# Optimization experiments

Measured on AMD Instinct MI355X. Metric: run time of the kernel, lower is better.

## Reference

```python
import jax, jax.numpy as jnp
import numpy as np

B, S = 256, 512
NQ = 1000           # n_skills
MEM, DK, DV, FC = 20, 50, 200, 50  # memory_size, key dim, value dim, final fc dim


def _kaiming(key, shape, fan_in):
    return jax.random.normal(key, shape) * np.float32(np.sqrt(2.0 / fan_in))


def setup_inputs() -> dict:
    key = jax.random.key(0)
    ks = jax.random.split(key, 12)
    q_data = jax.random.randint(ks[0], (B, S), 0, NQ + 1)
    qa_data = jax.random.randint(ks[1], (B, S), 0, 2 * NQ + 1)
    u = jax.random.uniform(ks[2], (B * S,))
    # target: -1 = masked/padding, else binary label (matches target.ge(0) masking)
    target = jnp.where(u < 0.1, -1.0, (u > 0.55).astype(jnp.float32))
    q_embed_w = _kaiming(ks[3], (NQ + 1, DK), DK)
    qa_embed_w = _kaiming(ks[4], (2 * NQ + 1, DV), DV)
    memory_key = _kaiming(ks[5], (MEM, DK), DK)
    init_memory_value = _kaiming(ks[6], (MEM, DV), DV)
    erase_w = _kaiming(ks[7], (DV, DV), DV)
    erase_b = jnp.zeros((DV,), jnp.float32)
    add_w = _kaiming(ks[8], (DV, DV), DV)
    add_b = jnp.zeros((DV,), jnp.float32)
    read_w = _kaiming(ks[9], (DV + FC, FC), DV + FC)
    read_b = jnp.zeros((FC,), jnp.float32)
    pred_w = _kaiming(ks[10], (FC, 1), FC)
    pred_b = jnp.zeros((1,), jnp.float32)
    return dict(q_data=q_data, qa_data=qa_data, target=target,
                q_embed_w=q_embed_w, qa_embed_w=qa_embed_w,
                memory_key=memory_key, init_memory_value=init_memory_value,
                erase_w=erase_w, erase_b=erase_b, add_w=add_w, add_b=add_b,
                read_w=read_w, read_b=read_b, pred_w=pred_w, pred_b=pred_b)


def reference(q_data, qa_data, target, q_embed_w, qa_embed_w, memory_key,
              init_memory_value, erase_w, erase_b, add_w, add_b,
              read_w, read_b, pred_w, pred_b):
    b = q_data.shape[0]
    q_e = q_embed_w[q_data]     # [B,S,DK]
    qa_e = qa_embed_w[qa_data]  # [B,S,DV]
    Mv0 = jnp.broadcast_to(init_memory_value, (b, MEM, DV))

    def step(Mv, xs):
        q_t, qa_t = xs                                        # [B,DK], [B,DV]
        corr = jax.nn.softmax(q_t @ memory_key.T, axis=1)     # [B,MEM] addressing
        read = jnp.einsum('bm,bmd->bd', corr, Mv)             # weighted read
        erase = jax.nn.sigmoid(qa_t @ erase_w + erase_b)      # [B,DV]
        add = jnp.tanh(qa_t @ add_w + add_b)                  # [B,DV]
        w = corr[:, :, None]                                  # [B,MEM,1]
        Mv = Mv * (1.0 - w * erase[:, None, :]) + w * add[:, None, :]
        return Mv, read

    _, reads = jax.lax.scan(step, Mv0, (q_e.transpose(1, 0, 2), qa_e.transpose(1, 0, 2)))
    reads = reads.transpose(1, 0, 2)                          # [B,S,DV]
    x = jnp.concatenate([reads, q_e], axis=-1)                # [B,S,DV+FC]
    h = jnp.tanh(x @ read_w + read_b)                         # [B,S,FC]
    logits = (h @ pred_w + pred_b).reshape(-1)                # [B*S]
    mask = target >= 0.0
    t = jnp.where(mask, target, 0.0)
    # numerically-stable BCE-with-logits, masked mean
    bce = jnp.maximum(logits, 0.0) - logits * t + jnp.log1p(jnp.exp(-jnp.abs(logits)))
    loss = jnp.sum(jnp.where(mask, bce, 0.0)) / jnp.maximum(mask.sum(), 1)
    return loss, jax.nn.sigmoid(logits)
```

## Files before the change

### kernel.cpp

```cpp
#include <hip/hip_runtime.h>
#include <math.h>

#define B_   256
#define S_   512
#define NQ_  1000
#define MEM_ 20
#define DK_  50
#define DV_  200
#define FC_  50
#define RPB  2
#define CHK  8
#define CLEN (S_/CHK)
#define HLEN 32
#define NKS  7
#define XS_STRIDE 232
#define CORR_STRIDE 12
#define NB_EA    ((2*NQ_+1+RPB-1)/RPB)
#define NB_CORR  4
#define NB_WPACK 7
#define NB_HQ    251
#define PREP_BLOCKS (NB_EA+NB_CORR+NB_WPACK+NB_HQ)
#define MM_BLOCKS (B_*CHK)
#define SCANA_BLOCKS (B_*(CHK-1))

typedef __attribute__((ext_vector_type(8))) short bf16x8_t;
typedef __attribute__((ext_vector_type(4))) float f32x4_t;
typedef __attribute__((ext_vector_type(2))) _Float16 f16x2_t;

static __device__ __forceinline__ f16x2_t h2(unsigned u){ return __builtin_bit_cast(f16x2_t, u); }
static __device__ __forceinline__ unsigned h2u(f16x2_t v){ return __builtin_bit_cast(unsigned, v); }
static __device__ __forceinline__ unsigned packh2(float x, float y){
  unsigned short bx = __builtin_bit_cast(unsigned short, (_Float16)x);
  unsigned short by = __builtin_bit_cast(unsigned short, (_Float16)y);
  return (unsigned)bx | ((unsigned)by << 16);
}
static __device__ __forceinline__ f16x2_t pkfma16(f16x2_t a, f16x2_t b, f16x2_t c){
  return __builtin_elementwise_fma(a, b, c);
}
static __device__ __forceinline__ f16x2_t splat_l(f16x2_t p){ return __builtin_shufflevector(p, p, 0, 0); }
static __device__ __forceinline__ f16x2_t splat_h(f16x2_t p){ return __builtin_shufflevector(p, p, 1, 1); }

static __device__ __forceinline__ unsigned short f2bf(float f){
  unsigned u = __float_as_uint(f);
  unsigned r = u + 0x7fffu + ((u >> 16) & 1u);
  return (unsigned short)(r >> 16);
}
static __device__ __forceinline__ float ftanh(float x){
  float e = __expf(2.f*x);
  return 1.f - 2.f*__builtin_amdgcn_rcpf(e+1.f);
}
static __device__ __forceinline__ float fsigm(float x){
  return __builtin_amdgcn_rcpf(1.f+__expf(-x));
}

__global__ __launch_bounds__(256) void k_prep1(
    const float* __restrict__ qaw,
    const float* __restrict__ ew, const float* __restrict__ eb,
    const float* __restrict__ aw, const float* __restrict__ ab,
    unsigned* __restrict__ eaTab,
    const float* __restrict__ qw, const float* __restrict__ mk,
    unsigned* __restrict__ corrH,
    const float* __restrict__ rw, const float* __restrict__ rb,
    const float* __restrict__ pw,
    unsigned short* __restrict__ WpFrag, float* __restrict__ pwPad,
    float* __restrict__ hq){
  __shared__ float qa[RPB*DV_];
  int blk = blockIdx.x;
  if(blk < NB_EA){
    int row0 = blk*RPB;
    for(int i=threadIdx.x; i<RPB*DV_; i+=256){
      int r = i/DV_, cc = i - r*DV_;
      int row = row0 + r;
      qa[i] = (row <= 2*NQ_) ? qaw[row*DV_+cc] : 0.f;
    }
    __syncthreads();
    int d = threadIdx.x;
    if(d >= DV_) return;
    float accE[RPB], accA[RPB];
    #pragma unroll
    for(int r=0;r<RPB;++r){ accE[r] = eb[d]; accA[r] = ab[d]; }
    float we0 = ew[d], wa0 = aw[d];
    for(int j=0;j<DV_;++j){
      int jn = (j+1 < DV_) ? j+1 : j;
      float we1 = ew[jn*DV_+d];
      float wa1 = aw[jn*DV_+d];
      #pragma unroll
      for(int r=0;r<RPB;++r){
        float x = qa[r*DV_+j];
        accE[r] = fmaf(x, we0, accE[r]);
        accA[r] = fmaf(x, wa0, accA[r]);
      }
      we0 = we1; wa0 = wa1;
    }
    #pragma unroll
    for(int r=0;r<RPB;++r){
      int row = row0 + r;
      if(row <= 2*NQ_){
        unsigned he = (unsigned)__builtin_bit_cast(unsigned short, (_Float16)fsigm(accE[r]));
        unsigned ha = (unsigned)__builtin_bit_cast(unsigned short, (_Float16)ftanh(accA[r]));
        eaTab[(size_t)row*DV_+d] = he | (ha << 16);
      }
    }
  } else if(blk < NB_EA+NB_CORR){
    int q = (blk-NB_EA)*256 + threadIdx.x;
    if(q > NQ_) return;
    float qv[DK_];
    #pragma unroll
    for(int j=0;j<DK_;++j) qv[j] = qw[q*DK_+j];
    float s[MEM_]; float mx = -1e30f;
    #pragma unroll
    for(int m=0;m<MEM_;++m){
      float acc = 0.f;
      #pragma unroll
      for(int j=0;j<DK_;++j) acc = fmaf(qv[j], mk[m*DK_+j], acc);
      s[m] = acc; mx = fmaxf(mx, acc);
    }
    float sum = 0.f;
    #pragma unroll
    for(int m=0;m<MEM_;++m){ s[m] = __expf(s[m]-mx); sum += s[m]; }
    float inv = __builtin_amdgcn_rcpf(sum);
    #pragma unroll
    for(int i=0;i<MEM_/2;++i)
      corrH[q*CORR_STRIDE+i] = packh2(s[2*i]*inv, s[2*i+1]*inv);
  } else if(blk < NB_EA+NB_CORR+NB_WPACK){
    int ks = blk - (NB_EA+NB_CORR);
    int nt = threadIdx.x >> 6;
    int lane = threadIdx.x & 63;
    int quad = lane >> 4, col = lane & 15;
    int n = nt*16 + col;
    unsigned short tmp[8];
    #pragma unroll
    for(int j=0;j<8;++j){
      int k = ks*32 + quad*8 + j;
      tmp[j] = (k < DV_ && n < FC_) ? f2bf(rw[k*FC_+n]) : (unsigned short)0;
    }
    uint4* dst = reinterpret_cast<uint4*>(WpFrag + ((size_t)(ks*4+nt)*64 + lane)*8);
    *dst = *reinterpret_cast<const uint4*>(tmp);
    if(ks == 0 && threadIdx.x < 64)
      pwPad[threadIdx.x] = (threadIdx.x < FC_) ? pw[threadIdx.x] : 0.f;
  } else {
    int idx = (blk-(NB_EA+NB_CORR+NB_WPACK))*256 + threadIdx.x;
    int q = idx >> 6, n = idx & 63;
    if(q > NQ_) return;
    float v = 0.f;
    if(n < FC_){
      float acc = rb[n];
      #pragma unroll
      for(int j=0;j<DK_;++j)
        acc = fmaf(qw[q*DK_+j], rw[(DV_+j)*FC_+n], acc);
      v = acc;
    }
    hq[q*64+n] = v;
  }
}

__global__ __launch_bounds__(256,8) void k_scanA(const int* __restrict__ qd,
    const int* __restrict__ qad,
    const unsigned* __restrict__ corrH,
    const unsigned* __restrict__ eaTab,
    unsigned* __restrict__ ABu){
  const int blk = blockIdx.x;
  const int b = blk / (CHK-1), c = blk % (CHK-1);
  const int d = threadIdx.x;
  const int dc = (d < DV_) ? d : DV_-1;
  const bool act = (d < DV_);
  const int* __restrict__ qp  = qd  + b*S_ + c*CLEN;
  const int* __restrict__ qap = qad + b*S_ + c*CLEN;

  const f16x2_t one2h = {(_Float16)1.f, (_Float16)1.f};
  f16x2_t A2[MEM_/2], B2[MEM_/2];
  #pragma unroll
  for(int i=0;i<MEM_/2;++i){ A2[i] = one2h; B2[i] = (f16x2_t){(_Float16)0.f,(_Float16)0.f}; }

  unsigned ea0 = eaTab[(size_t)qap[0]*DV_ + dc];
  unsigned ea1 = eaTab[(size_t)qap[1]*DV_ + dc];
  unsigned ea2 = eaTab[(size_t)qap[2]*DV_ + dc];
  int qa3 = qap[3], qa4 = qap[4], qa5 = qap[5];
  int s0 = __builtin_amdgcn_readfirstlane(qp[0]);
  int s1 = __builtin_amdgcn_readfirstlane(qp[1]);
  const unsigned* c0p = corrH + s0*CORR_STRIDE;
  uint4 ca0 = *(const uint4*)(c0p); uint4 cb0 = *(const uint4*)(c0p+4); uint2 cc0 = *(const uint2*)(c0p+8);
  const unsigned* c1p = corrH + s1*CORR_STRIDE;
  uint4 ca1 = *(const uint4*)(c1p); uint4 cb1 = *(const uint4*)(c1p+4); uint2 cc1 = *(const uint2*)(c1p+8);
  int qn2 = qp[2], qn3 = qp[3];

  #pragma unroll 4
  for(int t=0;t<CLEN;++t){
    int qs = __builtin_amdgcn_readfirstlane(qn2);
    const unsigned* cnp = corrH + qs*CORR_STRIDE;
    uint4 ca2 = *(const uint4*)(cnp);
    uint4 cb2 = *(const uint4*)(cnp+4);
    uint2 cc2 = *(const uint2*)(cnp+8);
    unsigned eanew = eaTab[(size_t)qa3*DV_ + dc];
    int t4 = (t+4 < CLEN) ? t+4 : CLEN-1;
    int qnew = qp[t4];
    int t6 = (t+6 < CLEN) ? t+6 : CLEN-1;
    int qanew = qap[t6];

    f16x2_t pe = h2(ea0);
    const f16x2_t ee = splat_l(pe), aa = splat_h(pe);
    #define UPDA(u, i) { \
      f16x2_t cp = h2(u); \
      f16x2_t al = pkfma16(-cp, ee, one2h); \
      f16x2_t be = cp*aa; \
      A2[i] = A2[i]*al; \
      B2[i] = pkfma16(al, B2[i], be); }
    UPDA(ca0.x, 0)  UPDA(ca0.y, 1)  UPDA(ca0.z, 2)  UPDA(ca0.w, 3)
    UPDA(cb0.x, 4)  UPDA(cb0.y, 5)  UPDA(cb0.z, 6)  UPDA(cb0.w, 7)
    UPDA(cc0.x, 8)  UPDA(cc0.y, 9)
    #undef UPDA

    ca0=ca1; cb0=cb1; cc0=cc1;
    ca1=ca2; cb1=cb2; cc1=cc2;
    qn2=qn3; qn3=qnew;
    ea0=ea1; ea1=ea2; ea2=eanew;
    qa3=qa4; qa4=qa5; qa5=qanew;
  }
  if(act){
    unsigned* base = ABu + ((size_t)(b*(CHK-1) + c)*MEM_)*DV_ + d;
    #pragma unroll
    for(int i=0;i<MEM_/2;++i){
      unsigned a01 = h2u(A2[i]);
      unsigned b01 = h2u(B2[i]);
      base[(size_t)(2*i)*DV_]   = (a01 & 0xffffu) | (b01 << 16);
      base[(size_t)(2*i+1)*DV_] = (a01 >> 16)     | (b01 & 0xffff0000u);
    }
  }
}

__global__ __launch_bounds__(256) void k_prefix(const float* __restrict__ mv0,
    const unsigned* __restrict__ ABu, unsigned* __restrict__ Mv0p){
  int i = blockIdx.x*256 + threadIdx.x;
  if(i >= B_*(MEM_/2)*DV_) return;
  int d = i % DV_;
  int p = (i / DV_) % (MEM_/2);
  int b = i / (DV_*(MEM_/2));
  float MvE = mv0[(2*p)*DV_+d];
  float MvO = mv0[(2*p+1)*DV_+d];
  #pragma unroll
  for(int c=1;c<CHK;++c){
    unsigned vE = ABu[((size_t)(b*(CHK-1) + (c-1))*MEM_ + 2*p)*DV_ + d];
    unsigned vO = ABu[((size_t)(b*(CHK-1) + (c-1))*MEM_ + 2*p+1)*DV_ + d];
    MvE = fmaf((float)h2(vE)[0], MvE, (float)h2(vE)[1]);
    MvO = fmaf((float)h2(vO)[0], MvO, (float)h2(vO)[1]);
    Mv0p[((size_t)(b*CHK + c)*(MEM_/2) + p)*DV_ + d] = packh2(MvE, MvO);
  }
}

__global__ __launch_bounds__(256,8) void k_scan_mm(const int* __restrict__ qd,
    const int* __restrict__ qad,
    const unsigned* __restrict__ corrH,
    const unsigned* __restrict__ eaTab,
    const float* __restrict__ mv0,
    const unsigned* __restrict__ Mv0p,
    const unsigned short* __restrict__ WpFrag,
    const float* __restrict__ hq,
    const float* __restrict__ pwPad, const float* __restrict__ pb,
    const float* __restrict__ target,
    float* __restrict__ out, float2* __restrict__ partials){
  __shared__ unsigned short Xs[CLEN*XS_STRIDE];
  __shared__ float sred[2][2][16];
  __shared__ float sbce[4];

  const int blk = blockIdx.x;
  const int b = blk >> 3, c8 = blk & (CHK-1);
  const int d = threadIdx.x;
  const int dc = (d < DV_) ? d : DV_-1;
  const bool act = (d < DV_);
  const bool padw = (d < 224);
  const int* __restrict__ qp  = qd  + b*S_ + c8*CLEN;
  const int* __restrict__ qap = qad + b*S_ + c8*CLEN;

  const int wave = threadIdx.x >> 6;
  const int lane = threadIdx.x & 63;
  const int col  = lane & 15, quad = lane >> 4;
  const int rt   = wave & 1;
  const int nh   = wave >> 1;
  const int mbase = rt*16;

  f16x2_t Mv2[MEM_/2];
  if(c8 == 0){
    #pragma unroll
    for(int i=0;i<MEM_/2;++i)
      Mv2[i] = (f16x2_t){ (_Float16)mv0[(2*i)*DV_+dc], (_Float16)mv0[(2*i+1)*DV_+dc] };
  } else {
    const unsigned* base = Mv0p + ((size_t)(b*CHK + c8)*(MEM_/2))*DV_ + dc;
    #pragma unroll
    for(int i=0;i<MEM_/2;++i)
      Mv2[i] = h2(base[(size_t)i*DV_]);
  }

  unsigned ea0 = eaTab[(size_t)qap[0]*DV_ + dc];
  unsigned ea1 = eaTab[(size_t)qap[1]*DV_ + dc];
  unsigned ea2 = eaTab[(size_t)qap[2]*DV_ + dc];
  int qa3 = qap[3], qa4 = qap[4], qa5 = qap[5];
  int s0 = __builtin_amdgcn_readfirstlane(qp[0]);
  int s1 = __builtin_amdgcn_readfirstlane(qp[1]);
  const unsigned* c0p = corrH + s0*CORR_STRIDE;
  uint4 ca0 = *(const uint4*)(c0p); uint4 cb0 = *(const uint4*)(c0p+4); uint2 cc0 = *(const uint2*)(c0p+8);
  const unsigned* c1p = corrH + s1*CORR_STRIDE;
  uint4 ca1 = *(const uint4*)(c1p); uint4 cb1 = *(const uint4*)(c1p+4); uint2 cc1 = *(const uint2*)(c1p+8);
  int qn2 = qp[2], qn3 = qp[3];

  #pragma unroll 4
  for(int t=0;t<CLEN;++t){
    int qs = __builtin_amdgcn_readfirstlane(qn2);
    const unsigned* cnp = corrH + qs*CORR_STRIDE;
    uint4 ca2 = *(const uint4*)(cnp);
    uint4 cb2 = *(const uint4*)(cnp+4);
    uint2 cc2 = *(const uint2*)(cnp+8);
    unsigned eanew = eaTab[(size_t)qa3*DV_ + dc];
    int t4 = (t+4 < CLEN) ? t+4 : CLEN-1;
    int qnew = qp[t4];
    int t6 = (t+6 < CLEN) ? t+6 : CLEN-1;
    int qanew = qap[t6];

    f16x2_t pe = h2(ea0);
    const f16x2_t ee = splat_l(pe), aa = splat_h(pe);
    float rd0 = 0.f, rd1 = 0.f;
    #define UPD2(u, i, acc) { \
      f16x2_t cp = h2(u); \
      acc = __builtin_amdgcn_fdot2(cp, Mv2[i], acc, false); \
      f16x2_t tt = pkfma16(-Mv2[i], ee, aa); \
      Mv2[i] = pkfma16(cp, tt, Mv2[i]); }
    UPD2(ca0.x, 0, rd0)  UPD2(ca0.y, 1, rd1)  UPD2(ca0.z, 2, rd0)  UPD2(ca0.w, 3, rd1)
    UPD2(cb0.x, 4, rd0)  UPD2(cb0.y, 5, rd1)  UPD2(cb0.z, 6, rd0)  UPD2(cb0.w, 7, rd1)
    UPD2(cc0.x, 8, rd0)  UPD2(cc0.y, 9, rd1)
    #undef UPD2

    if(padw) Xs[t*XS_STRIDE + d] = act ? f2bf(rd0+rd1) : (unsigned short)0;

    ca0=ca1; cb0=cb1; cc0=cc1;
    ca1=ca2; cb1=cb2; cc1=cc2;
    qn2=qn3; qn3=qnew;
    ea0=ea1; ea1=ea2; ea2=eanew;
    qa3=qa4; qa4=qa5; qa5=qanew;
  }
  __syncthreads();

  float bceAcc = 0.f, cntAcc = 0.f;
  const float pbv = pb[0];

  #pragma unroll
  for(int h=0;h<2;++h){
    const int g0 = h*HLEN;

    int qpre[4];
    #pragma unroll
    for(int reg=0;reg<4;++reg) qpre[reg] = qp[g0 + mbase + quad*4 + reg];
    float hqv[4][2];
    #pragma unroll
    for(int reg=0;reg<4;++reg)
      #pragma unroll
      for(int j=0;j<2;++j)
        hqv[reg][j] = hq[qpre[reg]*64 + (nh*2+j)*16 + col];

    f32x4_t acc[2];
    acc[0] = (f32x4_t){0.f,0.f,0.f,0.f};
    acc[1] = (f32x4_t){0.f,0.f,0.f,0.f};
    #pragma unroll
    for(int ks=0;ks<NKS;++ks){
      bf16x8_t a = *reinterpret_cast<const bf16x8_t*>(Xs + (g0 + mbase + col)*XS_STRIDE + quad*8 + ks*32);
      #pragma unroll
      for(int j=0;j<2;++j){
        int nt = nh*2 + j;
        bf16x8_t bfr = *reinterpret_cast<const bf16x8_t*>(WpFrag + ((size_t)(ks*4+nt)*64 + lane)*8);
        acc[j] = __builtin_amdgcn_mfma_f32_16x16x32_bf16(a, bfr, acc[j], 0, 0, 0);
      }
    }

    float part[4];
    #pragma unroll
    for(int reg=0;reg<4;++reg){
      float s = 0.f;
      #pragma unroll
      for(int j=0;j<2;++j){
        int n = (nh*2+j)*16 + col;
        float hh = acc[j][reg] + hqv[reg][j];
        s = fmaf(pwPad[n], ftanh(hh), s);
      }
      part[reg] = s;
    }
    #pragma unroll
    for(int off=1; off<16; off<<=1){
      #pragma unroll
      for(int reg=0;reg<4;++reg) part[reg] += __shfl_xor(part[reg], off, 64);
    }
    if(col == 0){
      #pragma unroll
      for(int reg=0;reg<4;++reg) sred[rt][nh][quad*4+reg] = part[reg];
    }
    __syncthreads();

    if(nh == 0 && col == 0){
      #pragma unroll
      for(int reg=0;reg<4;++reg){
        int idx = quad*4 + reg;
        int mloc = mbase + idx;
        int row = b*S_ + c8*CLEN + g0 + mloc;
        float logit = sred[rt][0][idx] + sred[rt][1][idx] + pbv;
        out[1+row] = fsigm(logit);
        float t = target[row];
        if(t >= 0.f){
          cntAcc += 1.f;
          bceAcc += fmaxf(logit,0.f) - logit*t + log1pf(__expf(-fabsf(logit)));
        }
      }
    }
    __syncthreads();
  }

  bceAcc += __shfl_xor(bceAcc, 16, 64); cntAcc += __shfl_xor(cntAcc, 16, 64);
  bceAcc += __shfl_xor(bceAcc, 32, 64); cntAcc += __shfl_xor(cntAcc, 32, 64);
  if(lane == 0 && nh == 0){ sbce[wave] = bceAcc; sbce[2+wave] = cntAcc; }
  __syncthreads();
  if(threadIdx.x == 0)
    partials[blk] = make_float2(sbce[0]+sbce[1], sbce[2]+sbce[3]);
}

__global__ __launch_bounds__(256) void k_fin(const float2* __restrict__ partials,
                                             float* __restrict__ out){
  float bce = 0.f, cnt = 0.f;
  for(int i=threadIdx.x; i<MM_BLOCKS; i+=256){
    float2 p = partials[i];
    bce += p.x; cnt += p.y;
  }
  #pragma unroll
  for(int off=32; off>0; off>>=1){
    bce += __shfl_down(bce, off, 64);
    cnt += __shfl_down(cnt, off, 64);
  }
  __shared__ float sb[4], sc[4];
  int w = threadIdx.x >> 6;
  if((threadIdx.x & 63) == 0){ sb[w] = bce; sc[w] = cnt; }
  __syncthreads();
  if(threadIdx.x == 0){
    float Bt = sb[0]+sb[1]+sb[2]+sb[3];
    float Ct = sc[0]+sc[1]+sc[2]+sc[3];
    out[0] = Bt / fmaxf(Ct, 1.f);
  }
}

extern "C" void kernel_launch(void* const* d_in, const int* in_sizes, int n_in,
                              void* d_out, int out_size, void* d_ws, size_t ws_size,
                              hipStream_t stream){
  const int*   qd     = (const int*)d_in[0];
  const int*   qad    = (const int*)d_in[1];
  const float* target = (const float*)d_in[2];
  const float* qw     = (const float*)d_in[3];
  const float* qaw    = (const float*)d_in[4];
  const float* mk     = (const float*)d_in[5];
  const float* mv0    = (const float*)d_in[6];
  const float* ew     = (const float*)d_in[7];
  const float* eb     = (const float*)d_in[8];
  const float* aw     = (const float*)d_in[9];
  const float* ab     = (const float*)d_in[10];
  const float* rw     = (const float*)d_in[11];
  const float* rb     = (const float*)d_in[12];
  const float* pw     = (const float*)d_in[13];
  const float* pb     = (const float*)d_in[14];
  float* out = (float*)d_out;

  char* ws = (char*)d_ws;
  size_t off = 0;
  float2* partials = (float2*)(ws + off);            off += (size_t)MM_BLOCKS*8;
  unsigned* corrH = (unsigned*)(ws + off);           off += (((size_t)(NQ_+1)*CORR_STRIDE*4 + 255)/256)*256;
  unsigned* eaTab = (unsigned*)(ws + off);           off += (((size_t)(2*NQ_+1)*DV_*4 + 255)/256)*256;
  unsigned* ABu   = (unsigned*)(ws + off);           off += (size_t)SCANA_BLOCKS*MEM_*DV_*4;
  unsigned* Mv0p  = (unsigned*)(ws + off);           off += (size_t)MM_BLOCKS*(MEM_/2)*DV_*4;
  unsigned short* WpFrag = (unsigned short*)(ws + off); off += ((size_t)NKS*4*64*8*2 + 255)/256*256;
  float* pwPad    = (float*)(ws + off);              off += 256;
  float* hq       = (float*)(ws + off);              off += (size_t)(NQ_+1)*64*4;

  k_prep1<<<dim3(PREP_BLOCKS), dim3(256), 0, stream>>>(qaw, ew, eb, aw, ab, eaTab,
                                                       qw, mk, corrH,
                                                       rw, rb, pw, WpFrag, pwPad, hq);
  k_scanA<<<dim3(SCANA_BLOCKS), dim3(256), 0, stream>>>(qd, qad, corrH, eaTab, ABu);
  k_prefix<<<dim3((B_*(MEM_/2)*DV_+255)/256), dim3(256), 0, stream>>>(mv0, ABu, Mv0p);
  k_scan_mm<<<dim3(MM_BLOCKS), dim3(256), 0, stream>>>(qd, qad, corrH, eaTab,
                                                       mv0, Mv0p, WpFrag, hq, pwPad, pb, target, out, partials);
  k_fin<<<dim3(1), dim3(256), 0, stream>>>(partials, out);
}
```

Measured before the change: 215.6 us.

## Compute erase/add table with fp16 MFMA tiles in prep kernel

The per-answer erase/add projection table (2001x200 times two 200x200 weights) was computed with scalar FMAs, two rows per block. It now uses 32x64 output tiles staged in LDS as fp16 and 16x16x32 f16 MFMA instructions, with the A fragments held in registers and reused for both weight matrices. This cuts the prep kernel's scalar arithmetic and repeated weight reads. In exchange the matmul inputs are rounded to fp16 before accumulation, which lowers precision slightly.

```diff
diff --git a/kernel.cpp b/kernel.cpp
--- a/kernel.cpp
+++ b/kernel.cpp
@@ -8,22 +8,22 @@
 #define DK_  50
 #define DV_  200
 #define FC_  50
-#define RPB  2
 #define CHK  8
 #define CLEN (S_/CHK)
 #define HLEN 32
 #define NKS  7
 #define XS_STRIDE 232
 #define CORR_STRIDE 12
-#define NB_EA    ((2*NQ_+1+RPB-1)/RPB)
+#define NB_EAMM  252
 #define NB_CORR  4
 #define NB_WPACK 7
 #define NB_HQ    251
-#define PREP_BLOCKS (NB_EA+NB_CORR+NB_WPACK+NB_HQ)
+#define PREP_BLOCKS (NB_EAMM+NB_CORR+NB_WPACK+NB_HQ)
 #define MM_BLOCKS (B_*CHK)
 #define SCANA_BLOCKS (B_*(CHK-1))
 
 typedef __attribute__((ext_vector_type(8))) short bf16x8_t;
+typedef __attribute__((ext_vector_type(8))) _Float16 f16x8_t;
 typedef __attribute__((ext_vector_type(4))) float f32x4_t;
 typedef __attribute__((ext_vector_type(2))) _Float16 f16x2_t;
 
@@ -64,45 +64,95 @@
     const float* __restrict__ pw,
     unsigned short* __restrict__ WpFrag, float* __restrict__ pwPad,
     float* __restrict__ hq){
-  __shared__ float qa[RPB*DV_];
+  __shared__ __align__(16) _Float16 sh[(32+64)*232];
   int blk = blockIdx.x;
-  if(blk < NB_EA){
-    int row0 = blk*RPB;
-    for(int i=threadIdx.x; i<RPB*DV_; i+=256){
-      int r = i/DV_, cc = i - r*DV_;
-      int row = row0 + r;
-      qa[i] = (row <= 2*NQ_) ? qaw[row*DV_+cc] : 0.f;
+  int td = threadIdx.x;
+  if(blk < NB_EAMM){
+    _Float16* qaL = sh;
+    _Float16* bL  = sh + 32*232;
+    const int rt = blk >> 2, ct = blk & 3;
+    const int row0 = rt*32, n0 = ct*64;
+
+    #pragma unroll
+    for(int i=0;i<28;++i){
+      int idx = td + 256*i;
+      int m = (int)(((unsigned)idx*37450u)>>23);
+      int k = idx - m*224;
+      int row = row0 + m;
+      float v = (k < DV_ && row <= 2*NQ_) ? qaw[(size_t)row*DV_ + k] : 0.f;
+      qaL[m*232 + k] = (_Float16)v;
     }
     __syncthreads();
-    int d = threadIdx.x;
-    if(d >= DV_) return;
-    float accE[RPB], accA[RPB];
-    #pragma unroll
-    for(int r=0;r<RPB;++r){ accE[r] = eb[d]; accA[r] = ab[d]; }
-    float we0 = ew[d], wa0 = aw[d];
-    for(int j=0;j<DV_;++j){
-      int jn = (j+1 < DV_) ? j+1 : j;
-      float we1 = ew[jn*DV_+d];
-      float wa1 = aw[jn*DV_+d];
-      #pragma unroll
-      for(int r=0;r<RPB;++r){
-        float x = qa[r*DV_+j];
-        accE[r] = fmaf(x, we0, accE[r]);
-        accA[r] = fmaf(x, wa0, accA[r]);
+
+    const int lane = td & 63, wave = td >> 6;
+    const int col = lane & 15, quad = lane >> 4;
+    const int mt = wave >> 1;
+    const int ntA = (wave & 1)*2;
+
+    f16x8_t afr[NKS];
+    #pragma unroll
+    for(int ks=0;ks<NKS;++ks)
+      afr[ks] = *(const f16x8_t*)(qaL + (mt*16+col)*232 + quad*8 + ks*32);
+
+    #pragma unroll
+    for(int i=0;i<56;++i){
+      int idx = td + 256*i;
+      int k = idx >> 6, n = idx & 63;
+      int ng = n0 + n;
+      float v = (k < DV_ && ng < DV_) ? ew[(size_t)k*DV_ + ng] : 0.f;
+      bL[n*232 + k] = (_Float16)v;
+    }
+    __syncthreads();
+    f32x4_t accE[2];
+    accE[0] = (f32x4_t){0.f,0.f,0.f,0.f};
+    accE[1] = (f32x4_t){0.f,0.f,0.f,0.f};
+    #pragma unroll
+    for(int ks=0;ks<NKS;++ks){
+      f16x8_t b0 = *(const f16x8_t*)(bL + ((ntA+0)*16+col)*232 + quad*8 + ks*32);
+      f16x8_t b1 = *(const f16x8_t*)(bL + ((ntA+1)*16+col)*232 + quad*8 + ks*32);
+      accE[0] = __builtin_amdgcn_mfma_f32_16x16x32_f16(afr[ks], b0, accE[0], 0, 0, 0);
+      accE[1] = __builtin_amdgcn_mfma_f32_16x16x32_f16(afr[ks], b1, accE[1], 0, 0, 0);
+    }
+    __syncthreads();
+
+    #pragma unroll
+    for(int i=0;i<56;++i){
+      int idx = td + 256*i;
+      int k = idx >> 6, n = idx & 63;
+      int ng = n0 + n;
+      float v = (k < DV_ && ng < DV_) ? aw[(size_t)k*DV_ + ng] : 0.f;
+      bL[n*232 + k] = (_Float16)v;
+    }
+    __syncthreads();
+    f32x4_t accA[2];
+    accA[0] = (f32x4_t){0.f,0.f,0.f,0.f};
+    accA[1] = (f32x4_t){0.f,0.f,0.f,0.f};
+    #pragma unroll
+    for(int ks=0;ks<NKS;++ks){
+      f16x8_t b0 = *(const f16x8_t*)(bL + ((ntA+0)*16+col)*232 + quad*8 + ks*32);
+      f16x8_t b1 = *(const f16x8_t*)(bL + ((ntA+1)*16+col)*232 + quad*8 + ks*32);
+      accA[0] = __builtin_amdgcn_mfma_f32_16x16x32_f16(afr[ks], b0, accA[0], 0, 0, 0);
+      accA[1] = __builtin_amdgcn_mfma_f32_16x16x32_f16(afr[ks], b1, accA[1], 0, 0, 0);
+    }
+
+    #pragma unroll
+    for(int j=0;j<2;++j){
+      int ng = n0 + (ntA+j)*16 + col;
+      if(ng < DV_){
+        float ebv = eb[ng], abv = ab[ng];
+        #pragma unroll
+        for(int reg=0;reg<4;++reg){
+          int row = row0 + mt*16 + quad*4 + reg;
+          if(row <= 2*NQ_){
+            float e = fsigm(accE[j][reg] + ebv);
+            float a = ftanh(accA[j][reg] + abv);
+            eaTab[(size_t)row*DV_ + ng] = packh2(e, a);
+          }
+        }
       }
-      we0 = we1; wa0 = wa1;
-    }
-    #pragma unroll
-    for(int r=0;r<RPB;++r){
-      int row = row0 + r;
-      if(row <= 2*NQ_){
-        unsigned he = (unsigned)__builtin_bit_cast(unsigned short, (_Float16)fsigm(accE[r]));
-        unsigned ha = (unsigned)__builtin_bit_cast(unsigned short, (_Float16)ftanh(accA[r]));
-        eaTab[(size_t)row*DV_+d] = he | (ha << 16);
-      }
-    }
-  } else if(blk < NB_EA+NB_CORR){
-    int q = (blk-NB_EA)*256 + threadIdx.x;
+    }
+  } else if(blk < NB_EAMM+NB_CORR){
+    int q = (blk-NB_EAMM)*256 + td;
     if(q > NQ_) return;
     float qv[DK_];
     #pragma unroll
@@ -122,10 +172,10 @@
     #pragma unroll
     for(int i=0;i<MEM_/2;++i)
       corrH[q*CORR_STRIDE+i] = packh2(s[2*i]*inv, s[2*i+1]*inv);
-  } else if(blk < NB_EA+NB_CORR+NB_WPACK){
-    int ks = blk - (NB_EA+NB_CORR);
-    int nt = threadIdx.x >> 6;
-    int lane = threadIdx.x & 63;
+  } else if(blk < NB_EAMM+NB_CORR+NB_WPACK){
+    int ks = blk - (NB_EAMM+NB_CORR);
+    int nt = td >> 6;
+    int lane = td & 63;
     int quad = lane >> 4, col = lane & 15;
     int n = nt*16 + col;
     unsigned short tmp[8];
@@ -136,10 +186,10 @@
     }
     uint4* dst = reinterpret_cast<uint4*>(WpFrag + ((size_t)(ks*4+nt)*64 + lane)*8);
     *dst = *reinterpret_cast<const uint4*>(tmp);
-    if(ks == 0 && threadIdx.x < 64)
-      pwPad[threadIdx.x] = (threadIdx.x < FC_) ? pw[threadIdx.x] : 0.f;
+    if(ks == 0 && td < 64)
+      pwPad[td] = (td < FC_) ? pw[td] : 0.f;
   } else {
-    int idx = (blk-(NB_EA+NB_CORR+NB_WPACK))*256 + threadIdx.x;
+    int idx = (blk-(NB_EAMM+NB_CORR+NB_WPACK))*256 + td;
     int q = idx >> 6, n = idx & 63;
     if(q > NQ_) return;
     float v = 0.f;
```

Result: slower. 231.1 us (+7.2%).
